# Optimization experiments

Hardware: AMD Instinct MI355X
Metric: run time of the kernel (lower is better)

Reference implementation:

```python
import jax, jax.numpy as jnp
import numpy as np
from jax import lax

HD = 64      # head_dim
PS = 2       # fine patch size
EPS = 1e-5   # batchnorm eps

def _conv(x, w, stride, pad, groups=1):
    return lax.conv_general_dilated(x, w, (stride, stride), ((pad, pad), (pad, pad)),
                                    feature_group_count=groups,
                                    dimension_numbers=('NCHW', 'OIHW', 'NCHW'))

def _conv_transpose(x, w, stride, pad):
    # torch ConvTranspose2d(in,out,k,stride,pad) with w [in,out,k,k]
    k = w.shape[-1]
    wt = jnp.flip(w, (2, 3)).transpose(1, 0, 2, 3)  # -> [out,in,k,k]
    e = k - 1 - pad
    return lax.conv_general_dilated(x, wt, (1, 1), ((e, e), (e, e)),
                                    lhs_dilation=(stride, stride),
                                    dimension_numbers=('NCHW', 'OIHW', 'NCHW'))

def _bn(x, g, b, m, v):
    inv = g / jnp.sqrt(v + EPS)
    return x * inv[None, :, None, None] + (b - m * inv)[None, :, None, None]

def setup_inputs() -> dict:
    key = jax.random.key(0)
    ks = jax.random.split(key, 12)
    B, C, H, W = 8, 256, 64, 64
    f = lambda k, sh, s=0.05: jax.random.normal(k, sh, jnp.float32) * s
    return {
        'x': jax.random.normal(ks[0], (B, C, H, W), jnp.float32),
        'down_w': f(ks[1], (C, C, 4, 4), 0.02), 'down_b': f(ks[2], (C,)),
        'up_w': f(ks[3], (C, C, 4, 4), 0.02), 'up_b': f(ks[4], (C,)),
        'wqkv_c': f(ks[5], (HD, 3 * HD)), 'bqkv_c': f(ks[6], (3 * HD,)),
        'wqkv_f': f(ks[7], (HD, 3 * HD)), 'bqkv_f': f(ks[8], (3 * HD,)),
        'dw_w': f(ks[9], (C, 1, 3, 3)),
        'bn1_g': jnp.ones((C,), jnp.float32), 'bn1_b': jnp.zeros((C,), jnp.float32),
        'bn1_m': jnp.zeros((C,), jnp.float32), 'bn1_v': jnp.ones((C,), jnp.float32),
        'pw_w': f(ks[10], (C, C, 1, 1)),
        'bn2_g': jnp.ones((C,), jnp.float32), 'bn2_b': jnp.zeros((C,), jnp.float32),
        'bn2_m': jnp.zeros((C,), jnp.float32), 'bn2_v': jnp.ones((C,), jnp.float32),
    }

def reference(x, down_w, down_b, up_w, up_b, wqkv_c, bqkv_c, wqkv_f, bqkv_f, dw_w,
              bn1_g, bn1_b, bn1_m, bn1_v, pw_w, bn2_g, bn2_b, bn2_m, bn2_v):
    B, C, H, W = x.shape
    nh = C // HD
    scale = HD ** -0.5

    # ---- CoarseSelfAttention: downsample -> per-head MHSA -> top-k -> upsample ----
    xd = _conv(x, down_w, 2, 1) + down_b[None, :, None, None]          # [B,C,H/2,W/2]
    h, w = H // 2, W // 2
    N = h * w
    tok = xd.reshape(B, nh, HD, N).transpose(0, 1, 3, 2)               # [B,nh,N,hd]
    q, k, v = jnp.split(tok @ wqkv_c + bqkv_c, 3, axis=-1)
    attn = jax.nn.softmax(jnp.einsum('bhnd,bhmd->bhnm', q, k) * scale, axis=-1)
    score = attn.sum(axis=-2)                                          # [B,nh,N]
    kf = max(1, N // 4)
    topk = lax.top_k(score, kf)[1]                                     # [B,nh,kf] int32
    out = jnp.einsum('bhnm,bhmd->bhnd', attn, v)
    out = out.transpose(0, 1, 3, 2).reshape(B, C, h, w)
    coarse = _conv_transpose(out, up_w, 2, 1) + up_b[None, :, None, None]  # [B,C,H,W]
    # F.interpolate to (H,W) is identity here: upsample output already matches x.

    # ---- TopkSelfAttention: gather top-k 2x2 patches, local MHSA, scatter back ----
    ph, pw = H // PS, W // PS
    xh = coarse.reshape(B, nh, HD, ph, PS, pw, PS)
    patches = xh.transpose(0, 1, 2, 3, 5, 4, 6).reshape(B, nh, HD, ph * pw, PS, PS)
    sel = jnp.take_along_axis(patches, topk[:, :, None, :, None, None], axis=3)  # [B,nh,hd,kf,PS,PS]
    tok_f = sel.reshape(B, nh, HD, kf, PS * PS).transpose(0, 1, 3, 4, 2).reshape(B, nh, kf * PS * PS, HD)
    qf, kfp, vf = jnp.split(tok_f @ wqkv_f + bqkv_f, 3, axis=-1)
    attn_f = jax.nn.softmax(jnp.einsum('bhnd,bhmd->bhnm', qf, kfp) * scale, axis=-1)
    out_f = jnp.einsum('bhnm,bhmd->bhnd', attn_f, vf)                  # [B,nh,kf*4,hd]
    out_p = out_f.reshape(B, nh, kf, PS * PS, HD).transpose(0, 1, 2, 4, 3).reshape(B, nh, kf, HD, PS, PS)
    bi = jnp.arange(B)[:, None, None]
    hi = jnp.arange(nh)[None, :, None]
    res = jnp.zeros_like(patches).at[bi, hi, :, topk].set(out_p)       # scatter (indices unique)
    region = res.reshape(B, nh, HD, ph, pw, PS, PS).transpose(0, 1, 2, 3, 5, 4, 6).reshape(B, C, H, W)

    # ---- residual + DWConv (depthwise->BN->ReLU6->pointwise->BN->ReLU6) ----
    y = coarse + region
    y = jnp.clip(_bn(_conv(y, dw_w, 1, 1, groups=C), bn1_g, bn1_b, bn1_m, bn1_v), 0.0, 6.0)
    y = jnp.clip(_bn(_conv(y, pw_w, 1, 0), bn2_g, bn2_b, bn2_m, bn2_v), 0.0, 6.0)
    return y
```

## Files before the change

### kernel.cpp

```cpp
#include <hip/hip_runtime.h>
#include <hip/hip_bf16.h>

typedef __hip_bfloat16 bf16;
typedef __bf16 bf16x8 __attribute__((ext_vector_type(8)));
typedef float f32x4 __attribute__((ext_vector_type(4)));


#define OFF_XDHWC    0L
#define OFF_QH       2097152L
#define OFF_T1       0L
#define OFF_OUTC     8388608L
#define OFF_COARSE   10485760L
#define OFF_XHL      10485760L
#define OFF_PSCW     10485760L
#define OFF_SCORE    19398656L
#define OFF_TOPK     19431424L
#define OFF_DOWNW    19439616L
#define OFF_DOWNWL   19963904L
#define OFF_UPW4     20488192L
#define OFF_WQKVC    21536768L
#define OFF_BQKVC    21549056L
#define OFF_WQKVF    21549248L
#define OFF_BQKVF    21561536L
#define OFF_PWW      21561728L
#define OFF_DWW      21627264L
#define OFF_BN1S     21629568L
#define OFF_BN1T     21629824L
#define OFF_BN2S     21630080L
#define OFF_BN2T     21630336L
#define OFF_DOWNB    21630592L
#define OFF_UPB      21630848L
#define OFF_FLAG     21631104L
#define WS_FLOATS    21631360L

__device__ __forceinline__ float relu6(float v) { return v < 0.f ? 0.f : (v > 6.f ? 6.f : v); }

__device__ __forceinline__ float ldin(const void* p, long i, int flag) {
    return flag ? __bfloat162float(((const bf16*)p)[i]) : ((const float*)p)[i];
}

__device__ __forceinline__ unsigned short f2bf(float f) {
    unsigned int b = __float_as_uint(f);
    b += 0x7FFFu + ((b >> 16) & 1u);
    return (unsigned short)(b >> 16);
}

__global__ __launch_bounds__(256) void detect_kernel(const void* __restrict__ x, int* __restrict__ flag) {
    __shared__ int cnt[256];
    int tid = threadIdx.x;
    int c = 0;
    for (int i = tid; i < 4096; i += 256) {
        long idx = (long)i * 2047;
        float v = __bfloat162float(((const bf16*)x)[idx]);
        float a = fabsf(v);
        if (isfinite(v) && a > 1e-8f && a < 100.f) c++;
    }
    cnt[tid] = c; __syncthreads();
    for (int s = 128; s > 0; s >>= 1) { if (tid < s) cnt[tid] += cnt[tid + s]; __syncthreads(); }
    if (tid == 0 && cnt[0] >= 3686) *flag = 1;
}

__global__ __launch_bounds__(256) void cvt_kernel(const void* __restrict__ in, float* __restrict__ out,
                                                  int n, const int* __restrict__ flagp) {
    int flag = *flagp;
    int i = blockIdx.x * 256 + threadIdx.x;
    if (i < n) out[i] = ldin(in, i, flag);
}

__global__ __launch_bounds__(256) void cvt_bf16_kernel(const void* __restrict__ in, unsigned short* __restrict__ out,
                                                       int n, const int* __restrict__ flagp) {
    int flag = *flagp;
    int i = blockIdx.x * 256 + threadIdx.x;
    if (i < n) out[i] = f2bf(ldin(in, i, flag));
}

__global__ __launch_bounds__(256) void split_pack_kernel(const void* __restrict__ in, unsigned int* __restrict__ out,
                                                         int n, const int* __restrict__ flagp) {
    int flag = *flagp;
    int i = blockIdx.x * 256 + threadIdx.x;
    if (i < n) {
        float v = ldin(in, i, flag);
        unsigned short h = f2bf(v);
        float fh = __uint_as_float(((unsigned int)h) << 16);
        unsigned short l = f2bf(v - fh);
        out[i] = (unsigned int)h | ((unsigned int)l << 16);
    }
}

__global__ __launch_bounds__(256) void split_kernel(const void* __restrict__ in,
                                                    unsigned short* __restrict__ hi, unsigned short* __restrict__ lo,
                                                    int n, const int* __restrict__ flagp) {
    int flag = *flagp;
    int i = blockIdx.x * 256 + threadIdx.x;
    if (i < n) {
        float v = ldin(in, i, flag);
        unsigned short h = f2bf(v);
        float fh = __uint_as_float(((unsigned int)h) << 16);
        hi[i] = h;
        lo[i] = f2bf(v - fh);
    }
}

__global__ __launch_bounds__(256) void tqkv_kernel(const void* __restrict__ w, float* __restrict__ wt,
                                                   const int* __restrict__ flagp) {
    int flag = *flagp;
    int idx = blockIdx.x * 256 + threadIdx.x;
    if (idx >= 192 * 64) return;
    int j = idx >> 6, d = idx & 63;
    wt[idx] = ldin(w, d * 192 + j, flag);
}

__global__ __launch_bounds__(256) void prep_up_kernel(const void* __restrict__ w, unsigned short* __restrict__ W4,
                                                      const int* __restrict__ flagp) {
    int flag = *flagp;
    int idx = blockIdx.x * 256 + threadIdx.x;
    int cls = idx >> 18; int rem = idx & 262143;
    int co = rem >> 10; int q = rem & 1023;
    int ci = q >> 2; int j = q & 3;
    int pa = cls >> 1, pb = cls & 1;
    int jy = j >> 1, jx = j & 1;
    int ky = (pa == 0) ? (jy ? 3 : 1) : (jy ? 0 : 2);
    int kx = (pb == 0) ? (jx ? 3 : 1) : (jx ? 0 : 2);
    W4[idx] = f2bf(ldin(w, (((long)ci * 256 + co) * 4 + ky) * 4 + kx, flag));
}

__global__ void bn_prep_kernel(const void* __restrict__ g, const void* __restrict__ b,
                               const void* __restrict__ m, const void* __restrict__ v,
                               float* __restrict__ s, float* __restrict__ t,
                               const int* __restrict__ flagp) {
    int flag = *flagp;
    int c = threadIdx.x;
    float gv = ldin(g, c, flag), bv = ldin(b, c, flag);
    float mv = ldin(m, c, flag), vv = ldin(v, c, flag);
    float inv = gv / sqrtf(vv + 1e-5f);
    s[c] = inv; t[c] = bv - mv * inv;
}

__global__ __launch_bounds__(256) void gemm_mfma_x2(
    const unsigned int* __restrict__ XHL,
    const unsigned short* __restrict__ WH, const unsigned short* __restrict__ WL,
    float* __restrict__ C, const float* __restrict__ e0)
{
    __shared__ __align__(16) unsigned short Ah[64 * 40];
    __shared__ __align__(16) unsigned short Al[64 * 40];
    __shared__ __align__(16) unsigned short Bh[64 * 40];
    __shared__ __align__(16) unsigned short Bl[64 * 40];
    int m0 = blockIdx.y * 64, n0 = blockIdx.x * 64;
    int tid = threadIdx.x;
    int w = tid >> 6, l = tid & 63, l15 = l & 15, q = l >> 4;

    int offA[8], ldsA[8];
    #pragma unroll
    for (int i = 0; i < 8; i++) {
        int idx = i * 256 + tid;
        int kl = idx & 31, ml = idx >> 5;
        int m = m0 + ml;
        int b = m >> 10, oy = (m >> 5) & 31, ox = m & 31;
        int c0 = kl >> 4;
        int ky = (kl >> 2) & 3, kx = kl & 3;
        int iy = 2 * oy - 1 + ky, ix = 2 * ox - 1 + kx;
        ldsA[i] = ml * 40 + kl;
        offA[i] = ((unsigned)iy < 64u && (unsigned)ix < 64u)
                  ? (((b * 256 + c0) * 64 + iy) * 64 + ix) : -1;
    }
    unsigned int aR[8];
    uint4 bhR, blR;
    int bn = tid >> 2, bk = (tid & 3) * 8;

    auto loadA = [&](int k0) {
        int cb = (k0 >> 4) * 4096;
        #pragma unroll
        for (int i = 0; i < 8; i++)
            aR[i] = (offA[i] >= 0) ? XHL[offA[i] + cb] : 0u;
    };
    auto storeA = [&]() {
        #pragma unroll
        for (int i = 0; i < 8; i++) {
            Ah[ldsA[i]] = (unsigned short)(aR[i] & 0xffffu);
            Al[ldsA[i]] = (unsigned short)(aR[i] >> 16);
        }
    };
    auto loadB = [&](int k0) {
        bhR = *(const uint4*)(WH + (long)(n0 + bn) * 4096 + (k0 + bk));
        blR = *(const uint4*)(WL + (long)(n0 + bn) * 4096 + (k0 + bk));
    };

    f32x4 acc[4] = {};
    loadA(0); loadB(0);
    for (int k0 = 0; k0 < 4096; k0 += 32) {
        storeA();
        *(uint4*)(&Bh[bn * 40 + bk]) = bhR;
        *(uint4*)(&Bl[bn * 40 + bk]) = blR;
        __syncthreads();
        if (k0 + 32 < 4096) { loadA(k0 + 32); loadB(k0 + 32); }
        bf16x8 afh = *(const bf16x8*)(&Ah[(w * 16 + l15) * 40 + q * 8]);
        bf16x8 afl = *(const bf16x8*)(&Al[(w * 16 + l15) * 40 + q * 8]);
        #pragma unroll
        for (int j4 = 0; j4 < 4; j4++) {
            bf16x8 bfh = *(const bf16x8*)(&Bh[(j4 * 16 + l15) * 40 + q * 8]);
            bf16x8 bfl = *(const bf16x8*)(&Bl[(j4 * 16 + l15) * 40 + q * 8]);
            acc[j4] = __builtin_amdgcn_mfma_f32_16x16x32_bf16(afh, bfh, acc[j4], 0, 0, 0);
            acc[j4] = __builtin_amdgcn_mfma_f32_16x16x32_bf16(afh, bfl, acc[j4], 0, 0, 0);
            acc[j4] = __builtin_amdgcn_mfma_f32_16x16x32_bf16(afl, bfh, acc[j4], 0, 0, 0);
        }
        __syncthreads();
    }
    #pragma unroll
    for (int j4 = 0; j4 < 4; j4++) {
        int n = n0 + j4 * 16 + l15;
        #pragma unroll
        for (int r = 0; r < 4; r++) {
            int m = m0 + w * 16 + q * 4 + r;
            C[(long)m * 256 + n] = acc[j4][r] + e0[n];
        }
    }
}

template<int EPI>
__global__ __launch_bounds__(256) void gemm_k(
    const float* __restrict__ A, const float* __restrict__ B,
    unsigned short* __restrict__ out, int K, int sAm, int sBn, const float* __restrict__ e0)
{
    __shared__ float As[16][68];
    __shared__ float Bs[16][68];
    int m0 = blockIdx.y * 64;
    int n0 = blockIdx.x * 64;
    int tid = threadIdx.x;
    int tx = tid & 15, ty = tid >> 4;
    int l4 = tid >> 2, kq = (tid & 3) * 4;
    float4 aR, bR;

    auto loadA = [&](int k0) { aR = *(const float4*)(A + (long)(m0 + l4) * sAm + (k0 + kq)); };
    auto loadB = [&](int k0) { bR = *(const float4*)(B + (long)(n0 + l4) * sBn + (k0 + kq)); };

    float acc[4][4] = {};
    loadA(0); loadB(0);
    for (int k0 = 0; k0 < K; k0 += 16) {
        As[kq + 0][l4] = aR.x; As[kq + 1][l4] = aR.y; As[kq + 2][l4] = aR.z; As[kq + 3][l4] = aR.w;
        Bs[kq + 0][l4] = bR.x; Bs[kq + 1][l4] = bR.y; Bs[kq + 2][l4] = bR.z; Bs[kq + 3][l4] = bR.w;
        __syncthreads();
        if (k0 + 16 < K) { loadA(k0 + 16); loadB(k0 + 16); }
        #pragma unroll
        for (int kk = 0; kk < 16; ++kk) {
            float4 av = *reinterpret_cast<const float4*>(&As[kk][ty * 4]);
            float4 bv = *reinterpret_cast<const float4*>(&Bs[kk][tx * 4]);
            float a[4] = {av.x, av.y, av.z, av.w};
            float b[4] = {bv.x, bv.y, bv.z, bv.w};
            #pragma unroll
            for (int i = 0; i < 4; i++)
                #pragma unroll
                for (int j = 0; j < 4; j++)
                    acc[i][j] += a[i] * b[j];
        }
        __syncthreads();
    }
    #pragma unroll
    for (int i = 0; i < 4; i++) {
        int m = m0 + ty * 4 + i;
        int bh, tok;
        if (EPI == 2) { int bi = m >> 12; int h = m & 3; tok = (m >> 2) & 1023; bh = bi * 4 + h; }
        else          { bh = m >> 10; tok = m & 1023; }
        #pragma unroll
        for (int j = 0; j < 4; j++) {
            int n = n0 + tx * 4 + j;
            float v = acc[i][j] + e0[n];
            if (n < 64) {
                v *= 0.125f;
                unsigned short hb = f2bf(v);
                float fh = __uint_as_float(((unsigned int)hb) << 16);
                unsigned short lb = f2bf(v - fh);
                long p = (((long)bh << 10) + tok) * 64 + n;
                out[p] = hb; out[p + 2097152] = lb;
            } else if (n < 128) {
                unsigned short hb = f2bf(v);
                float fh = __uint_as_float(((unsigned int)hb) << 16);
                unsigned short lb = f2bf(v - fh);
                long p = (((long)bh << 10) + tok) * 64 + (n - 64);
                out[p + 4194304] = hb; out[p + 6291456] = lb;
            } else {
                out[8388608 + (((long)bh << 6) + (n - 128)) * 1024 + tok] = f2bf(v);
            }
        }
    }
}

template<int EPI, int AMODE>
__global__ __launch_bounds__(256) void gemm_mfma(
    const float* __restrict__ A, const unsigned short* __restrict__ Bb, float* __restrict__ C,
    int K, long sAz, long sBz, int sAk, int sBn,
    const float* __restrict__ e0, const float* __restrict__ e1,
    void* __restrict__ ob, const int* __restrict__ flagp)
{
    __shared__ __align__(16) unsigned short Asb[64 * 40];
    __shared__ __align__(16) unsigned short Bsb[64 * 40];
    int z = blockIdx.z;
    if (AMODE == 0) A += (long)z * sAz;
    Bb += (long)z * sBz;
    int m0 = blockIdx.y * 64, n0 = blockIdx.x * 64;
    int tid = threadIdx.x;
    int w = tid >> 6, l = tid & 63;
    int l15 = l & 15, q = l >> 4;
    float aR[8];
    uint4 bR;

    auto loadA = [&](int k0) {
        if (AMODE == 0) {
            #pragma unroll
            for (int i = 0; i < 8; i++) {
                int idx = i * 256 + tid;
                int ml = idx & 63, kl = idx >> 6;
                aR[i] = A[(long)(k0 + kl) * sAk + (m0 + ml)];
            }
        } else {
            #pragma unroll
            for (int i = 0; i < 8; i++) {
                int idx = i * 256 + tid;
                int kl = idx & 31, ml = idx >> 5;
                int m = m0 + ml, k = k0 + kl;
                int b = m >> 10, y = (m >> 5) & 31, x2 = m & 31;
                int ci = k >> 2, j = k & 3;
                int pa = z >> 1, pb = z & 1;
                int jy = j >> 1, jx = j & 1;
                int dy = (pa == 0) ? (jy ? -1 : 0) : (jy ? 1 : 0);
                int dx = (pb == 0) ? (jx ? -1 : 0) : (jx ? 1 : 0);
                int yy = y + dy, xx = x2 + dx;
                float val = 0.f;
                if ((unsigned)yy < 32u && (unsigned)xx < 32u)
                    val = A[(((long)b * 4 + (ci >> 6)) * 1024 + yy * 32 + xx) * 64 + (ci & 63)];
                aR[i] = val;
            }
        }
    };
    auto storeA = [&]() {
        #pragma unroll
        for (int i = 0; i < 8; i++) {
            int idx = i * 256 + tid;
            int ml, kl;
            if (AMODE == 0) { ml = idx & 63; kl = idx >> 6; }
            else            { kl = idx & 31; ml = idx >> 5; }
            Asb[ml * 40 + kl] = f2bf(aR[i]);
        }
    };
    int bn = tid >> 2, bk = (tid & 3) * 8;
    auto loadB = [&](int k0) {
        bR = *(const uint4*)(Bb + (long)(n0 + bn) * sBn + (k0 + bk));
    };

    f32x4 acc[4] = {};
    loadA(0); loadB(0);
    for (int k0 = 0; k0 < K; k0 += 32) {
        storeA();
        *(uint4*)(&Bsb[bn * 40 + bk]) = bR;
        __syncthreads();
        if (k0 + 32 < K) { loadA(k0 + 32); loadB(k0 + 32); }
        bf16x8 af = *(const bf16x8*)(&Asb[(w * 16 + l15) * 40 + q * 8]);
        #pragma unroll
        for (int j4 = 0; j4 < 4; j4++) {
            bf16x8 bf = *(const bf16x8*)(&Bsb[(j4 * 16 + l15) * 40 + q * 8]);
            acc[j4] = __builtin_amdgcn_mfma_f32_16x16x32_bf16(af, bf, acc[j4], 0, 0, 0);
        }
        __syncthreads();
    }
    int oflag = (EPI == 5) ? *flagp : 0;
    #pragma unroll
    for (int j4 = 0; j4 < 4; j4++) {
        int n = n0 + j4 * 16 + l15;
        #pragma unroll
        for (int r = 0; r < 4; r++) {
            int m = m0 + w * 16 + q * 4 + r;
            float v = acc[j4][r];
            if (EPI == 4) {
                v += e0[n];
                int pa = z >> 1, pb = z & 1;
                int bi = m >> 10, y = (m >> 5) & 31, x2 = m & 31;
                C[(((long)bi * 256 + n) * 64 + (2 * y + pa)) * 64 + (2 * x2 + pb)] = v;
            } else {
                v = relu6(v * e0[n] + e1[n]);
                long oidx = (long)z * 1048576 + (long)n * 4096 + m;
                if (oflag) ((bf16*)ob)[oidx] = __float2bfloat16(v);
                else       ((float*)ob)[oidx] = v;
            }
        }
    }
}

template<bool SCORE>
__global__ __launch_bounds__(256) void attn_mfma(
    const unsigned short* __restrict__ P0,
    float* __restrict__ O, float* __restrict__ PSCW)
{
    const unsigned short* QH = P0;
    const unsigned short* QL = P0 + 2097152;
    const unsigned short* KH = P0 + 4194304;
    const unsigned short* KL = P0 + 6291456;
    const unsigned short* VT = P0 + 8388608;
    __shared__ __align__(16) unsigned short Khs[64 * 72];
    __shared__ __align__(16) unsigned short Kls[64 * 72];
    __shared__ __align__(16) unsigned short Vs[64 * 72];
    __shared__ __align__(16) unsigned short Ps[4][16 * 72];
    int bh = blockIdx.y, rt = blockIdx.x;
    int tid = threadIdx.x;
    int w = tid >> 6, l = tid & 63, l15 = l & 15, q = l >> 4;

    long qoff = (((long)bh << 10) + rt * 64 + w * 16 + l15) * 64 + q * 8;
    bf16x8 afh[2], afl[2];
    afh[0] = *(const bf16x8*)(QH + qoff);
    afh[1] = *(const bf16x8*)(QH + qoff + 32);
    afl[0] = *(const bf16x8*)(QL + qoff);
    afl[1] = *(const bf16x8*)(QL + qoff + 32);

    float mr[4], lr[4];
    #pragma unroll
    for (int r = 0; r < 4; r++) { mr[r] = -1e30f; lr[r] = 0.f; }
    f32x4 o[4] = {};

    auto stageK = [&](int t) {
        #pragma unroll
        for (int i = 0; i < 2; i++) {
            int u = tid + i * 256;
            int tok = u >> 3, dp = (u & 7) * 8;
            long g = (((long)bh << 10) + t * 64 + tok) * 64 + dp;
            *(uint4*)(Khs + tok * 72 + dp) = *(const uint4*)(KH + g);
            *(uint4*)(Kls + tok * 72 + dp) = *(const uint4*)(KL + g);
        }
    };
    auto stageV = [&](int t) {
        #pragma unroll
        for (int i = 0; i < 2; i++) {
            int u = tid + i * 256;
            int d = u >> 3, k0 = (u & 7) * 8;
            long g = (((long)bh << 6) + d) * 1024 + t * 64 + k0;
            *(uint4*)(Vs + d * 72 + k0) = *(const uint4*)(VT + g);
        }
    };
    auto computeS = [&](f32x4* s) {
        #pragma unroll
        for (int kk = 0; kk < 2; kk++)
            #pragma unroll
            for (int j4 = 0; j4 < 4; j4++) {
                bf16x8 kh8 = *(const bf16x8*)(&Khs[(j4 * 16 + l15) * 72 + kk * 32 + q * 8]);
                bf16x8 kl8 = *(const bf16x8*)(&Kls[(j4 * 16 + l15) * 72 + kk * 32 + q * 8]);
                s[j4] = __builtin_amdgcn_mfma_f32_16x16x32_bf16(afh[kk], kh8, s[j4], 0, 0, 0);
                s[j4] = __builtin_amdgcn_mfma_f32_16x16x32_bf16(afh[kk], kl8, s[j4], 0, 0, 0);
                s[j4] = __builtin_amdgcn_mfma_f32_16x16x32_bf16(afl[kk], kh8, s[j4], 0, 0, 0);
            }
    };
    auto pv = [&]() {
        #pragma unroll
        for (int kk = 0; kk < 2; kk++) {
            bf16x8 ap = *(const bf16x8*)(&Ps[w][l15 * 72 + kk * 32 + q * 8]);
            #pragma unroll
            for (int j4 = 0; j4 < 4; j4++) {
                bf16x8 bv = *(const bf16x8*)(&Vs[(j4 * 16 + l15) * 72 + kk * 32 + q * 8]);
                o[j4] = __builtin_amdgcn_mfma_f32_16x16x32_bf16(ap, bv, o[j4], 0, 0, 0);
            }
        }
    };

    if (SCORE) {
        for (int t = 0; t < 16; ++t) {
            __syncthreads();
            stageK(t);
            __syncthreads();
            f32x4 s[4] = {};
            computeS(s);
            #pragma unroll
            for (int r = 0; r < 4; r++) {
                float tm = fmaxf(fmaxf(s[0][r], s[1][r]), fmaxf(s[2][r], s[3][r]));
                #pragma unroll
                for (int off = 1; off < 16; off <<= 1) tm = fmaxf(tm, __shfl_xor(tm, off));
                float mn = fmaxf(mr[r], tm);
                float ss = __expf(s[0][r] - mn) + __expf(s[1][r] - mn)
                         + __expf(s[2][r] - mn) + __expf(s[3][r] - mn);
                #pragma unroll
                for (int off = 1; off < 16; off <<= 1) ss += __shfl_xor(ss, off);
                lr[r] = lr[r] * __expf(mr[r] - mn) + ss;
                mr[r] = mn;
            }
        }
        float linv[4];
        #pragma unroll
        for (int r = 0; r < 4; r++) linv[r] = 1.f / lr[r];
        for (int t = 0; t < 16; ++t) {
            __syncthreads();
            stageK(t); stageV(t);
            __syncthreads();
            f32x4 s[4] = {};
            computeS(s);
            float cs[4] = {0.f, 0.f, 0.f, 0.f};
            #pragma unroll
            for (int j4 = 0; j4 < 4; j4++)
                #pragma unroll
                for (int r = 0; r < 4; r++) {
                    float p = __expf(s[j4][r] - mr[r]) * linv[r];
                    cs[j4] += p;
                    Ps[w][(q * 4 + r) * 72 + j4 * 16 + l15] = f2bf(p);
                }
            #pragma unroll
            for (int j4 = 0; j4 < 4; j4++) {
                cs[j4] += __shfl_xor(cs[j4], 16);
                cs[j4] += __shfl_xor(cs[j4], 32);
            }
            if (q == 0) {
                long pb = (((long)(bh * 16 + rt) * 4 + w) << 10) + t * 64;
                #pragma unroll
                for (int j4 = 0; j4 < 4; j4++) PSCW[pb + j4 * 16 + l15] = cs[j4];
            }
            __syncthreads();
            pv();
        }
    } else {
        for (int t = 0; t < 16; ++t) {
            __syncthreads();
            stageK(t); stageV(t);
            __syncthreads();
            f32x4 s[4] = {};
            computeS(s);
            float corr[4];
            #pragma unroll
            for (int r = 0; r < 4; r++) {
                float tm = fmaxf(fmaxf(s[0][r], s[1][r]), fmaxf(s[2][r], s[3][r]));
                #pragma unroll
                for (int off = 1; off < 16; off <<= 1) tm = fmaxf(tm, __shfl_xor(tm, off));
                float mn = fmaxf(mr[r], tm);
                corr[r] = __expf(mr[r] - mn);
                mr[r] = mn;
            }
            float ssr[4] = {0.f, 0.f, 0.f, 0.f};
            #pragma unroll
            for (int j4 = 0; j4 < 4; j4++)
                #pragma unroll
                for (int r = 0; r < 4; r++) {
                    float p = __expf(s[j4][r] - mr[r]);
                    ssr[r] += p;
                    Ps[w][(q * 4 + r) * 72 + j4 * 16 + l15] = f2bf(p);
                }
            #pragma unroll
            for (int r = 0; r < 4; r++) {
                float ss = ssr[r];
                #pragma unroll
                for (int off = 1; off < 16; off <<= 1) ss += __shfl_xor(ss, off);
                lr[r] = lr[r] * corr[r] + ss;
            }
            #pragma unroll
            for (int j4 = 0; j4 < 4; j4++)
                #pragma unroll
                for (int r = 0; r < 4; r++) o[j4][r] *= corr[r];
            __syncthreads();
            pv();
        }
    }

    float fin[4];
    #pragma unroll
    for (int r = 0; r < 4; r++) fin[r] = SCORE ? 1.f : (1.f / lr[r]);
    long obase = (((long)bh << 10) + rt * 64 + w * 16 + q * 4) * 64;
    #pragma unroll
    for (int j4 = 0; j4 < 4; j4++)
        #pragma unroll
        for (int r = 0; r < 4; r++)
            O[obase + (long)r * 64 + j4 * 16 + l15] = o[j4][r] * fin[r];
}

__global__ __launch_bounds__(256) void score_reduce_kernel(const float* __restrict__ PSCW, float* __restrict__ score) {
    int idx = blockIdx.x * 256 + threadIdx.x;
    int bh = idx >> 10, c = idx & 1023;
    float s = 0.f;
    for (int rw = 0; rw < 64; rw++) s += PSCW[(((long)bh * 64 + rw) << 10) + c];
    score[idx] = s;
}

__global__ __launch_bounds__(256) void topk_kernel(const float* __restrict__ score, int* __restrict__ topk) {
    __shared__ float s[1024];
    int z = blockIdx.x; int tid = threadIdx.x;
    for (int i = tid; i < 1024; i += 256) {
        float v = score[z * 1024 + i];
        s[i] = (v == v) ? v : -INFINITY;
    }
    __syncthreads();
    for (int i = tid; i < 1024; i += 256) {
        float si = s[i]; int r = 0;
        for (int j = 0; j < 1024; j++) {
            float sj = s[j];
            r += (sj > si) || (sj == si && j < i);
        }
        if (r < 256) topk[z * 256 + r] = i;
    }
}

__global__ __launch_bounds__(256) void gather_tokf_kernel(const float* __restrict__ coarse,
                                                          const int* __restrict__ topk,
                                                          float* __restrict__ tokf) {
    long idx = (long)blockIdx.x * 256 + threadIdx.x;
    int d = (int)(idx & 63); int t = (int)((idx >> 6) & 3);
    int j = (int)((idx >> 8) & 255); int bh = (int)(idx >> 16);
    int p = topk[bh * 256 + j] & 1023;
    int py = p >> 5, px = p & 31;
    int dy = t >> 1, dx = t & 1;
    int b = bh >> 2, h = bh & 3;
    tokf[idx] = coarse[(((long)b * 256 + h * 64 + d) * 64 + (2 * py + dy)) * 64 + (2 * px + dx)];
}

__global__ __launch_bounds__(256) void scatter_add_kernel(float* __restrict__ coarse,
                                                          const int* __restrict__ topk,
                                                          const float* __restrict__ outf) {
    long idx = (long)blockIdx.x * 256 + threadIdx.x;
    int d = (int)(idx & 63); int t = (int)((idx >> 6) & 3);
    int j = (int)((idx >> 8) & 255); int bh = (int)(idx >> 16);
    int p = topk[bh * 256 + j] & 1023;
    int py = p >> 5, px = p & 31;
    int dy = t >> 1, dx = t & 1;
    int b = bh >> 2, h = bh & 3;
    coarse[(((long)b * 256 + h * 64 + d) * 64 + (2 * py + dy)) * 64 + (2 * px + dx)] += outf[idx];
}

__global__ __launch_bounds__(64) void dw_bn_relu6_kernel(const float* __restrict__ y, const float* __restrict__ w9,
                                                         const float* __restrict__ s1, const float* __restrict__ t1,
                                                         float* __restrict__ out) {
    int gid = blockIdx.x;
    int row = gid & 63; int bc = gid >> 6; int c = bc & 255;
    int x = threadIdx.x;
    const float* base = y + (long)bc * 4096;
    float acc = 0.f;
    #pragma unroll
    for (int ky = 0; ky < 3; ky++) {
        int yy = row + ky - 1;
        if (yy < 0 || yy >= 64) continue;
        #pragma unroll
        for (int kx = 0; kx < 3; kx++) {
            int xx = x + kx - 1;
            if (xx < 0 || xx >= 64) continue;
            acc += base[yy * 64 + xx] * w9[c * 9 + ky * 3 + kx];
        }
    }
    out[(long)gid * 64 + x] = relu6(acc * s1[c] + t1[c]);
}

extern "C" void kernel_launch(void* const* d_in, const int* in_sizes, int n_in,
                              void* d_out, int out_size, void* d_ws, size_t ws_size,
                              hipStream_t stream) {
    if (ws_size < (size_t)WS_FLOATS * 4) return;

    const void* x      = d_in[0];
    const void* down_w = d_in[1];
    const void* down_b = d_in[2];
    const void* up_w   = d_in[3];
    const void* up_b   = d_in[4];
    const void* wqkv_c = d_in[5];
    const void* bqkv_c = d_in[6];
    const void* wqkv_f = d_in[7];
    const void* bqkv_f = d_in[8];
    const void* dw_w   = d_in[9];
    const void* bn1_g  = d_in[10];
    const void* bn1_b  = d_in[11];
    const void* bn1_m  = d_in[12];
    const void* bn1_v  = d_in[13];
    const void* pw_w   = d_in[14];
    const void* bn2_g  = d_in[15];
    const void* bn2_b  = d_in[16];
    const void* bn2_m  = d_in[17];
    const void* bn2_v  = d_in[18];

    float* ws = (float*)d_ws;
    int* flagp = (int*)(ws + OFF_FLAG);
    dim3 blk(256);

    hipMemsetAsync(flagp, 0, sizeof(int), stream);
    detect_kernel<<<1, blk, 0, stream>>>(x, flagp);

    split_pack_kernel<<<32768, blk, 0, stream>>>(x, (unsigned int*)(ws + OFF_XHL), 8388608, flagp);
    split_kernel<<<4096, blk, 0, stream>>>(down_w, (unsigned short*)(ws + OFF_DOWNW),
                                           (unsigned short*)(ws + OFF_DOWNWL), 1048576, flagp);
    cvt_kernel<<<1, blk, 0, stream>>>(down_b, ws + OFF_DOWNB, 256, flagp);
    cvt_kernel<<<1, blk, 0, stream>>>(up_b, ws + OFF_UPB, 256, flagp);
    cvt_kernel<<<1, blk, 0, stream>>>(bqkv_c, ws + OFF_BQKVC, 192, flagp);
    cvt_kernel<<<1, blk, 0, stream>>>(bqkv_f, ws + OFF_BQKVF, 192, flagp);
    cvt_bf16_kernel<<<256, blk, 0, stream>>>(pw_w, (unsigned short*)(ws + OFF_PWW), 65536, flagp);
    cvt_kernel<<<9, blk, 0, stream>>>(dw_w, ws + OFF_DWW, 2304, flagp);
    tqkv_kernel<<<48, blk, 0, stream>>>(wqkv_c, ws + OFF_WQKVC, flagp);
    tqkv_kernel<<<48, blk, 0, stream>>>(wqkv_f, ws + OFF_WQKVF, flagp);
    prep_up_kernel<<<4096, blk, 0, stream>>>(up_w, (unsigned short*)(ws + OFF_UPW4), flagp);
    bn_prep_kernel<<<1, blk, 0, stream>>>(bn1_g, bn1_b, bn1_m, bn1_v, ws + OFF_BN1S, ws + OFF_BN1T, flagp);
    bn_prep_kernel<<<1, blk, 0, stream>>>(bn2_g, bn2_b, bn2_m, bn2_v, ws + OFF_BN2S, ws + OFF_BN2T, flagp);

    gemm_mfma_x2<<<dim3(4, 128, 1), blk, 0, stream>>>((const unsigned int*)(ws + OFF_XHL),
        (const unsigned short*)(ws + OFF_DOWNW), (const unsigned short*)(ws + OFF_DOWNWL),
        ws + OFF_XDHWC, ws + OFF_DOWNB);

    gemm_k<2><<<dim3(3, 512, 1), blk, 0, stream>>>(ws + OFF_XDHWC, ws + OFF_WQKVC,
        (unsigned short*)(ws + OFF_QH), 64, 64, 64, ws + OFF_BQKVC);

    attn_mfma<true><<<dim3(16, 32), blk, 0, stream>>>((const unsigned short*)(ws + OFF_QH),
        ws + OFF_OUTC, ws + OFF_PSCW);
    score_reduce_kernel<<<128, blk, 0, stream>>>(ws + OFF_PSCW, ws + OFF_SCORE);
    topk_kernel<<<32, blk, 0, stream>>>(ws + OFF_SCORE, (int*)(ws + OFF_TOPK));

    gemm_mfma<4, 2><<<dim3(4, 128, 4), blk, 0, stream>>>(ws + OFF_OUTC, (unsigned short*)(ws + OFF_UPW4),
        ws + OFF_COARSE, 1024, 0, 262144, 0, 1024, ws + OFF_UPB, nullptr, nullptr, flagp);

    gather_tokf_kernel<<<8192, blk, 0, stream>>>(ws + OFF_COARSE, (const int*)(ws + OFF_TOPK), ws + OFF_XDHWC);
    gemm_k<3><<<dim3(3, 512, 1), blk, 0, stream>>>(ws + OFF_XDHWC, ws + OFF_WQKVF,
        (unsigned short*)(ws + OFF_QH), 64, 64, 64, ws + OFF_BQKVF);
    attn_mfma<false><<<dim3(16, 32), blk, 0, stream>>>((const unsigned short*)(ws + OFF_QH),
        ws + OFF_OUTC, nullptr);
    scatter_add_kernel<<<8192, blk, 0, stream>>>(ws + OFF_COARSE, (const int*)(ws + OFF_TOPK), ws + OFF_OUTC);

    dw_bn_relu6_kernel<<<131072, dim3(64), 0, stream>>>(ws + OFF_COARSE, ws + OFF_DWW,
        ws + OFF_BN1S, ws + OFF_BN1T, ws + OFF_T1);

    gemm_mfma<5, 0><<<dim3(4, 64, 8), blk, 0, stream>>>(ws + OFF_T1, (unsigned short*)(ws + OFF_PWW),
        nullptr, 256, 1048576, 0, 4096, 256, ws + OFF_BN2S, ws + OFF_BN2T, d_out, flagp);
}
```

Before: 803.9 us.

## Merge small prep kernels, fold score reduction into top-k, narrow down-conv GEMM tile

Ten tiny weight and bias conversion kernels are merged into one block-dispatched prep kernel, which removes launch overhead. The separate score-reduction kernel is folded into the top-k kernel. Each of its 32 blocks now sums 64 partial rows itself, so that step runs on far fewer threads than before. The down-sampling conv GEMM tile is narrowed from 64 to 32 output channels, doubling the grid to 1024 blocks for better occupancy, at the cost of reloading the A operand twice as often.

```diff
diff --git a/kernel.cpp b/kernel.cpp
--- a/kernel.cpp
+++ b/kernel.cpp
@@ -60,20 +60,6 @@
     if (tid == 0 && cnt[0] >= 3686) *flag = 1;
 }
 
-__global__ __launch_bounds__(256) void cvt_kernel(const void* __restrict__ in, float* __restrict__ out,
-                                                  int n, const int* __restrict__ flagp) {
-    int flag = *flagp;
-    int i = blockIdx.x * 256 + threadIdx.x;
-    if (i < n) out[i] = ldin(in, i, flag);
-}
-
-__global__ __launch_bounds__(256) void cvt_bf16_kernel(const void* __restrict__ in, unsigned short* __restrict__ out,
-                                                       int n, const int* __restrict__ flagp) {
-    int flag = *flagp;
-    int i = blockIdx.x * 256 + threadIdx.x;
-    if (i < n) out[i] = f2bf(ldin(in, i, flag));
-}
-
 __global__ __launch_bounds__(256) void split_pack_kernel(const void* __restrict__ in, unsigned int* __restrict__ out,
                                                          int n, const int* __restrict__ flagp) {
     int flag = *flagp;
@@ -99,15 +85,6 @@
         hi[i] = h;
         lo[i] = f2bf(v - fh);
     }
-}
-
-__global__ __launch_bounds__(256) void tqkv_kernel(const void* __restrict__ w, float* __restrict__ wt,
-                                                   const int* __restrict__ flagp) {
-    int flag = *flagp;
-    int idx = blockIdx.x * 256 + threadIdx.x;
-    if (idx >= 192 * 64) return;
-    int j = idx >> 6, d = idx & 63;
-    wt[idx] = ldin(w, d * 192 + j, flag);
 }
 
 __global__ __launch_bounds__(256) void prep_up_kernel(const void* __restrict__ w, unsigned short* __restrict__ W4,
@@ -124,16 +101,52 @@
     W4[idx] = f2bf(ldin(w, (((long)ci * 256 + co) * 4 + ky) * 4 + kx, flag));
 }
 
-__global__ void bn_prep_kernel(const void* __restrict__ g, const void* __restrict__ b,
-                               const void* __restrict__ m, const void* __restrict__ v,
-                               float* __restrict__ s, float* __restrict__ t,
-                               const int* __restrict__ flagp) {
+__global__ __launch_bounds__(256) void prep_misc_kernel(
+    const void* __restrict__ down_b, const void* __restrict__ up_b,
+    const void* __restrict__ bqkv_c, const void* __restrict__ bqkv_f,
+    const void* __restrict__ dw_w, const void* __restrict__ wqkv_c,
+    const void* __restrict__ wqkv_f, const void* __restrict__ pw_w,
+    const void* __restrict__ bn1_g, const void* __restrict__ bn1_b,
+    const void* __restrict__ bn1_m, const void* __restrict__ bn1_v,
+    const void* __restrict__ bn2_g, const void* __restrict__ bn2_b,
+    const void* __restrict__ bn2_m, const void* __restrict__ bn2_v,
+    float* __restrict__ ws, const int* __restrict__ flagp)
+{
     int flag = *flagp;
-    int c = threadIdx.x;
-    float gv = ldin(g, c, flag), bv = ldin(b, c, flag);
-    float mv = ldin(m, c, flag), vv = ldin(v, c, flag);
-    float inv = gv / sqrtf(vv + 1e-5f);
-    s[c] = inv; t[c] = bv - mv * inv;
+    int bid = blockIdx.x, tid = threadIdx.x;
+    if (bid < 48) {
+        int idx = bid * 256 + tid;
+        int j = idx >> 6, d = idx & 63;
+        ws[OFF_WQKVC + idx] = ldin(wqkv_c, d * 192 + j, flag);
+    } else if (bid < 96) {
+        int idx = (bid - 48) * 256 + tid;
+        int j = idx >> 6, d = idx & 63;
+        ws[OFF_WQKVF + idx] = ldin(wqkv_f, d * 192 + j, flag);
+    } else if (bid < 105) {
+        int i = (bid - 96) * 256 + tid;
+        if (i < 2304) ws[OFF_DWW + i] = ldin(dw_w, i, flag);
+    } else if (bid == 105) {
+        ws[OFF_DOWNB + tid] = ldin(down_b, tid, flag);
+    } else if (bid == 106) {
+        ws[OFF_UPB + tid] = ldin(up_b, tid, flag);
+    } else if (bid == 107) {
+        if (tid < 192) ws[OFF_BQKVC + tid] = ldin(bqkv_c, tid, flag);
+    } else if (bid == 108) {
+        if (tid < 192) ws[OFF_BQKVF + tid] = ldin(bqkv_f, tid, flag);
+    } else if (bid == 109) {
+        float gv = ldin(bn1_g, tid, flag), bv = ldin(bn1_b, tid, flag);
+        float mv = ldin(bn1_m, tid, flag), vv = ldin(bn1_v, tid, flag);
+        float inv = gv / sqrtf(vv + 1e-5f);
+        ws[OFF_BN1S + tid] = inv; ws[OFF_BN1T + tid] = bv - mv * inv;
+    } else if (bid == 110) {
+        float gv = ldin(bn2_g, tid, flag), bv = ldin(bn2_b, tid, flag);
+        float mv = ldin(bn2_m, tid, flag), vv = ldin(bn2_v, tid, flag);
+        float inv = gv / sqrtf(vv + 1e-5f);
+        ws[OFF_BN2S + tid] = inv; ws[OFF_BN2T + tid] = bv - mv * inv;
+    } else {
+        int i = (bid - 111) * 256 + tid;
+        ((unsigned short*)(ws + OFF_PWW))[i] = f2bf(ldin(pw_w, i, flag));
+    }
 }
 
 __global__ __launch_bounds__(256) void gemm_mfma_x2(
@@ -143,9 +156,9 @@
 {
     __shared__ __align__(16) unsigned short Ah[64 * 40];
     __shared__ __align__(16) unsigned short Al[64 * 40];
-    __shared__ __align__(16) unsigned short Bh[64 * 40];
-    __shared__ __align__(16) unsigned short Bl[64 * 40];
-    int m0 = blockIdx.y * 64, n0 = blockIdx.x * 64;
+    __shared__ __align__(16) unsigned short Bh[32 * 40];
+    __shared__ __align__(16) unsigned short Bl[32 * 40];
+    int m0 = blockIdx.y * 64, n0 = blockIdx.x * 32;
     int tid = threadIdx.x;
     int w = tid >> 6, l = tid & 63, l15 = l & 15, q = l >> 4;
 
@@ -164,8 +177,8 @@
                   ? (((b * 256 + c0) * 64 + iy) * 64 + ix) : -1;
     }
     unsigned int aR[8];
-    uint4 bhR, blR;
-    int bn = tid >> 2, bk = (tid & 3) * 8;
+    uint2 bhR, blR;
+    int bn = tid >> 3, bk = (tid & 7) * 4;
 
     auto loadA = [&](int k0) {
         int cb = (k0 >> 4) * 4096;
@@ -181,22 +194,22 @@
         }
     };
     auto loadB = [&](int k0) {
-        bhR = *(const uint4*)(WH + (long)(n0 + bn) * 4096 + (k0 + bk));
-        blR = *(const uint4*)(WL + (long)(n0 + bn) * 4096 + (k0 + bk));
-    };
-
-    f32x4 acc[4] = {};
+        bhR = *(const uint2*)(WH + (long)(n0 + bn) * 4096 + (k0 + bk));
+        blR = *(const uint2*)(WL + (long)(n0 + bn) * 4096 + (k0 + bk));
+    };
+
+    f32x4 acc[2] = {};
     loadA(0); loadB(0);
     for (int k0 = 0; k0 < 4096; k0 += 32) {
         storeA();
-        *(uint4*)(&Bh[bn * 40 + bk]) = bhR;
-        *(uint4*)(&Bl[bn * 40 + bk]) = blR;
+        *(uint2*)(&Bh[bn * 40 + bk]) = bhR;
+        *(uint2*)(&Bl[bn * 40 + bk]) = blR;
         __syncthreads();
         if (k0 + 32 < 4096) { loadA(k0 + 32); loadB(k0 + 32); }
         bf16x8 afh = *(const bf16x8*)(&Ah[(w * 16 + l15) * 40 + q * 8]);
         bf16x8 afl = *(const bf16x8*)(&Al[(w * 16 + l15) * 40 + q * 8]);
         #pragma unroll
-        for (int j4 = 0; j4 < 4; j4++) {
+        for (int j4 = 0; j4 < 2; j4++) {
             bf16x8 bfh = *(const bf16x8*)(&Bh[(j4 * 16 + l15) * 40 + q * 8]);
             bf16x8 bfl = *(const bf16x8*)(&Bl[(j4 * 16 + l15) * 40 + q * 8]);
             acc[j4] = __builtin_amdgcn_mfma_f32_16x16x32_bf16(afh, bfh, acc[j4], 0, 0, 0);
@@ -206,7 +219,7 @@
         __syncthreads();
     }
     #pragma unroll
-    for (int j4 = 0; j4 < 4; j4++) {
+    for (int j4 = 0; j4 < 2; j4++) {
         int n = n0 + j4 * 16 + l15;
         #pragma unroll
         for (int r = 0; r < 4; r++) {
@@ -562,19 +575,12 @@
             O[obase + (long)r * 64 + j4 * 16 + l15] = o[j4][r] * fin[r];
 }
 
-__global__ __launch_bounds__(256) void score_reduce_kernel(const float* __restrict__ PSCW, float* __restrict__ score) {
-    int idx = blockIdx.x * 256 + threadIdx.x;
-    int bh = idx >> 10, c = idx & 1023;
-    float s = 0.f;
-    for (int rw = 0; rw < 64; rw++) s += PSCW[(((long)bh * 64 + rw) << 10) + c];
-    score[idx] = s;
-}
-
-__global__ __launch_bounds__(256) void topk_kernel(const float* __restrict__ score, int* __restrict__ topk) {
+__global__ __launch_bounds__(256) void topk_kernel(const float* __restrict__ PSCW, int* __restrict__ topk) {
     __shared__ float s[1024];
     int z = blockIdx.x; int tid = threadIdx.x;
     for (int i = tid; i < 1024; i += 256) {
-        float v = score[z * 1024 + i];
+        float v = 0.f;
+        for (int rw = 0; rw < 64; rw++) v += PSCW[(((long)z * 64 + rw) << 10) + i];
         s[i] = (v == v) ? v : -INFINITY;
     }
     __syncthreads();
@@ -671,19 +677,12 @@
     split_pack_kernel<<<32768, blk, 0, stream>>>(x, (unsigned int*)(ws + OFF_XHL), 8388608, flagp);
     split_kernel<<<4096, blk, 0, stream>>>(down_w, (unsigned short*)(ws + OFF_DOWNW),
                                            (unsigned short*)(ws + OFF_DOWNWL), 1048576, flagp);
-    cvt_kernel<<<1, blk, 0, stream>>>(down_b, ws + OFF_DOWNB, 256, flagp);
-    cvt_kernel<<<1, blk, 0, stream>>>(up_b, ws + OFF_UPB, 256, flagp);
-    cvt_kernel<<<1, blk, 0, stream>>>(bqkv_c, ws + OFF_BQKVC, 192, flagp);
-    cvt_kernel<<<1, blk, 0, stream>>>(bqkv_f, ws + OFF_BQKVF, 192, flagp);
-    cvt_bf16_kernel<<<256, blk, 0, stream>>>(pw_w, (unsigned short*)(ws + OFF_PWW), 65536, flagp);
-    cvt_kernel<<<9, blk, 0, stream>>>(dw_w, ws + OFF_DWW, 2304, flagp);
-    tqkv_kernel<<<48, blk, 0, stream>>>(wqkv_c, ws + OFF_WQKVC, flagp);
-    tqkv_kernel<<<48, blk, 0, stream>>>(wqkv_f, ws + OFF_WQKVF, flagp);
+    prep_misc_kernel<<<367, blk, 0, stream>>>(down_b, up_b, bqkv_c, bqkv_f, dw_w, wqkv_c, wqkv_f, pw_w,
+                                              bn1_g, bn1_b, bn1_m, bn1_v, bn2_g, bn2_b, bn2_m, bn2_v,
+                                              ws, flagp);
     prep_up_kernel<<<4096, blk, 0, stream>>>(up_w, (unsigned short*)(ws + OFF_UPW4), flagp);
-    bn_prep_kernel<<<1, blk, 0, stream>>>(bn1_g, bn1_b, bn1_m, bn1_v, ws + OFF_BN1S, ws + OFF_BN1T, flagp);
-    bn_prep_kernel<<<1, blk, 0, stream>>>(bn2_g, bn2_b, bn2_m, bn2_v, ws + OFF_BN2S, ws + OFF_BN2T, flagp);
-
-    gemm_mfma_x2<<<dim3(4, 128, 1), blk, 0, stream>>>((const unsigned int*)(ws + OFF_XHL),
+
+    gemm_mfma_x2<<<dim3(8, 128, 1), blk, 0, stream>>>((const unsigned int*)(ws + OFF_XHL),
         (const unsigned short*)(ws + OFF_DOWNW), (const unsigned short*)(ws + OFF_DOWNWL),
         ws + OFF_XDHWC, ws + OFF_DOWNB);
 
@@ -692,8 +691,7 @@
 
     attn_mfma<true><<<dim3(16, 32), blk, 0, stream>>>((const unsigned short*)(ws + OFF_QH),
         ws + OFF_OUTC, ws + OFF_PSCW);
-    score_reduce_kernel<<<128, blk, 0, stream>>>(ws + OFF_PSCW, ws + OFF_SCORE);
-    topk_kernel<<<32, blk, 0, stream>>>(ws + OFF_SCORE, (int*)(ws + OFF_TOPK));
+    topk_kernel<<<32, blk, 0, stream>>>(ws + OFF_PSCW, (int*)(ws + OFF_TOPK));
 
     gemm_mfma<4, 2><<<dim3(4, 128, 4), blk, 0, stream>>>(ws + OFF_OUTC, (unsigned short*)(ws + OFF_UPW4),
         ws + OFF_COARSE, 1024, 0, 262144, 0, 1024, ws + OFF_UPB, nullptr, nullptr, flagp);
```

New measurement: 833.4 us. 1.04x slower.
